# Kernel tuning notes

Measured on AMD Instinct MI355X. Metric: run time of the kernel, lower is better.

The kernel has to match this reference:

```python
import jax, jax.numpy as jnp
import numpy as np

N_IMAGES = 2  # matches init kwarg


def setup_inputs() -> dict:
    key = jax.random.key(0)
    x = jax.random.normal(key, (8192, 128), dtype=jnp.float32)
    return {"x": x}


def reference(x):
    n_images = N_IMAGES
    N, D = x.shape
    P = N // n_images  # number of 'persons'
    G = x @ x.T  # [N, N] pairwise dot products (Gram matrix)

    # Offset pairs (i<j) within a window of n_images consecutive indices.
    # NB: original code uses range(person, person + n_images) -> sliding window.
    offs = np.array([(i, j) for i in range(n_images) for j in range(i + 1, n_images)])
    oi = jnp.asarray(offs[:, 0])  # [k]
    oj = jnp.asarray(offs[:, 1])  # [k]
    k = offs.shape[0]  # C(n_images, 2)

    p = jnp.arange(P)
    self_i = p[:, None] + oi[None, :]  # [P, k]
    self_j = p[:, None] + oj[None, :]  # [P, k]
    sim_self = jnp.min(G[self_i, self_j], axis=1)  # [P] min over self pairs

    # Upper-triangular (i<j) values; mask everything else to -inf.
    neg = jnp.finfo(G.dtype).min
    rows = jnp.arange(N)
    upper = jnp.where(rows[:, None] < rows[None, :], G, neg)

    # similarity_oth[p] = max over all i<j pairs excluding person p's k self pairs.
    # Only the global top-(k+1) values can ever be that max.
    top_vals, top_idx = jax.lax.top_k(upper.reshape(-1), k + 1)  # [k+1]
    self_flat = self_i * N + self_j  # [P, k] flat indices of self pairs
    member = (top_idx[None, :, None] == self_flat[:, None, :]).any(-1)  # [P, k+1]
    sim_oth = jnp.max(jnp.where(member, neg, top_vals[None, :]), axis=1)  # [P]

    return jnp.mean(sim_oth / sim_self)
```

## Files before the change

kernel.cpp:

```cpp
#include <hip/hip_runtime.h>
#include <hip/hip_bf16.h>
#include <math.h>
#include <float.h>

static constexpr int NN    = 8192;
static constexpr int DD    = 128;
static constexpr int PP    = 4096;
static constexpr int TILE  = 128;
static constexpr int TT    = NN / TILE;
static constexpr int NBLK  = TT * (TT + 1) / 2;
static constexpr int NC    = NBLK * 2;
static constexpr int GRP   = 1088;
static constexpr int TLDS  = 16 * GRP;

struct Cand { float v; unsigned idx; };

using short8 = __attribute__((ext_vector_type(8))) short;
using f32x4  = __attribute__((ext_vector_type(4))) float;

typedef const __attribute__((address_space(1))) unsigned int* gas_uint;
typedef __attribute__((address_space(3))) unsigned int* las_uint;

__device__ __forceinline__ void dma16(const void* g, const void* l) {
    __builtin_amdgcn_global_load_lds(
        (gas_uint)(unsigned long long)g,
        (las_uint)(unsigned)(unsigned long long)l, 16, 0, 0);
}

__device__ __forceinline__ unsigned pk2(float lo, float hi) {
    unsigned a = (unsigned)__builtin_bit_cast(unsigned short, __float2bfloat16(lo));
    unsigned b = (unsigned)__builtin_bit_cast(unsigned short, __float2bfloat16(hi));
    return a | (b << 16);
}

__device__ __forceinline__ void push1(float& v1, unsigned& i1, float& v2, unsigned& i2,
                                      float w, unsigned j) {
    if (w > v1) { v2 = v1; i2 = i1; v1 = w; i1 = j; }
    else if (w > v2) { v2 = w; i2 = j; }
}

__device__ __forceinline__ void merge2(float& v1, unsigned& i1, float& v2, unsigned& i2,
                                       float w1, unsigned j1, float w2, unsigned j2) {
    if (w1 > v1) {
        float nv2; unsigned ni2;
        if (v1 >= w2) { nv2 = v1; ni2 = i1; } else { nv2 = w2; ni2 = j2; }
        v1 = w1; i1 = j1; v2 = nv2; i2 = ni2;
    } else if (w1 > v2) {
        v2 = w1; i2 = j1;
    }
}

__global__ __launch_bounds__(256) void k_prep(const float* __restrict__ x,
                                              unsigned short* __restrict__ xb,
                                              double* __restrict__ ss) {
    const int tid = threadIdx.x;
    if (blockIdx.x < 256) {
        int chunk = blockIdx.x * 256 + tid;
        const float4* s = (const float4*)(x + (size_t)chunk * 16);
        float4 f0 = s[0], f1 = s[1], f2 = s[2], f3 = s[3];
        uint4 o0 = {pk2(f0.x, f0.y), pk2(f0.z, f0.w), pk2(f1.x, f1.y), pk2(f1.z, f1.w)};
        uint4 o1 = {pk2(f2.x, f2.y), pk2(f2.z, f2.w), pk2(f3.x, f3.y), pk2(f3.z, f3.w)};
        uint4* d = (uint4*)(xb + (size_t)chunk * 16);
        d[0] = o0; d[1] = o1;
    } else {
        int b = blockIdx.x - 256;
        const int wv = tid >> 6, lane = tid & 63;
        #pragma unroll 4
        for (int u = 0; u < 16; ++u) {
            int p = b * 64 + wv * 16 + u;
            const float* a  = x + (size_t)p * DD;
            const float* bb = a + DD;
            double s = (double)a[lane] * (double)bb[lane]
                     + (double)a[lane + 64] * (double)bb[lane + 64];
            #pragma unroll
            for (int off = 32; off >= 1; off >>= 1) s += __shfl_down(s, off);
            if (lane == 0) ss[p] = s;
        }
    }
}

__global__ __launch_bounds__(256, 4) void k_top2(const unsigned short* __restrict__ xb,
                                                 Cand* __restrict__ cands) {
    __shared__ __align__(16) char AsB[TLDS];
    __shared__ __align__(16) char BsB[TLDS];
    __shared__ float sv1[4], sv2[4];
    __shared__ unsigned si1[4], si2[4];

    const int tid  = threadIdx.x;
    const int wv   = tid >> 6;
    const int lane = tid & 63;

    int rem = blockIdx.x;
    int ti = 0;
    while (rem >= TT - ti) { rem -= (TT - ti); ++ti; }
    int tj = ti + rem;

    const int wm   = wv >> 1;
    const int wn   = wv & 1;
    const int quad = lane >> 4;
    const int r16  = lane & 15;

    const int grow = lane >> 3;
    const int gcol = (lane & 7) * 8;

    f32x4 acc[4][4];
    #pragma unroll
    for (int mi = 0; mi < 4; ++mi)
        #pragma unroll
        for (int nj = 0; nj < 4; ++nj)
            acc[mi][nj] = (f32x4){0.f, 0.f, 0.f, 0.f};

    #pragma unroll
    for (int p = 0; p < 2; ++p) {
        const int kk = p * 64;
        if (p) __syncthreads();

        #pragma unroll
        for (int t = 0; t < 4; ++t) {
            int g = wv * 4 + t;
            const unsigned short* ga =
                xb + (size_t)(ti * TILE + g * 8 + grow) * DD + kk + gcol;
            dma16(ga, AsB + g * GRP);
            const unsigned short* gb =
                xb + (size_t)(tj * TILE + g * 8 + grow) * DD + kk + gcol;
            dma16(gb, BsB + g * GRP);
        }
        __syncthreads();

        #pragma unroll
        for (int s = 0; s < 2; ++s) {
            const int cc = quad + 4 * s;
            short8 af[4], bfr[4];
            #pragma unroll
            for (int mi = 0; mi < 4; ++mi) {
                int ra = wm * 64 + mi * 16 + r16;
                af[mi] = *(const short8*)(AsB + (ra >> 3) * GRP + (ra & 7) * 128 + cc * 16);
                int rb = wn * 64 + mi * 16 + r16;
                bfr[mi] = *(const short8*)(BsB + (rb >> 3) * GRP + (rb & 7) * 128 + cc * 16);
            }
            #pragma unroll
            for (int mi = 0; mi < 4; ++mi)
                #pragma unroll
                for (int nj = 0; nj < 4; ++nj)
                    acc[mi][nj] = __builtin_amdgcn_mfma_f32_16x16x32_bf16(
                        af[mi], bfr[nj], acc[mi][nj], 0, 0, 0);
        }
    }

    const int ibase = ti * TILE + wm * 64;
    const int jbase = tj * TILE + wn * 64;
    float v1 = -INFINITY, v2 = -INFINITY;
    unsigned i1 = 0, i2 = 0;
    #pragma unroll
    for (int mi = 0; mi < 4; ++mi) {
        #pragma unroll
        for (int nj = 0; nj < 4; ++nj) {
            int gj = jbase + nj * 16 + r16;
            #pragma unroll
            for (int reg = 0; reg < 4; ++reg) {
                int gi = ibase + mi * 16 + quad * 4 + reg;
                if (gi < gj) {
                    unsigned idx = (unsigned)(gi * NN + gj);
                    push1(v1, i1, v2, i2, acc[mi][nj][reg], idx);
                }
            }
        }
    }

    #pragma unroll
    for (int off = 32; off >= 1; off >>= 1) {
        float    w1 = __shfl_down(v1, off);
        unsigned j1 = (unsigned)__shfl_down((int)i1, off);
        float    w2 = __shfl_down(v2, off);
        unsigned j2 = (unsigned)__shfl_down((int)i2, off);
        merge2(v1, i1, v2, i2, w1, j1, w2, j2);
    }
    if (lane == 0) { sv1[wv] = v1; si1[wv] = i1; sv2[wv] = v2; si2[wv] = i2; }
    __syncthreads();
    if (tid == 0) {
        for (int w = 1; w < 4; ++w)
            merge2(v1, i1, v2, i2, sv1[w], si1[w], sv2[w], si2[w]);
        cands[blockIdx.x * 2]     = {v1, i1};
        cands[blockIdx.x * 2 + 1] = {v2, i2};
    }
}

__global__ __launch_bounds__(256) void k_final(const float* __restrict__ x,
                                               const double* __restrict__ ss,
                                               const Cand* __restrict__ cands,
                                               float* __restrict__ out) {
    __shared__ float redv[8];
    __shared__ float s_thresh;
    __shared__ int cnt;
    __shared__ unsigned qidx[128];
    __shared__ double qex[128];
    __shared__ double sd1, sd2;
    __shared__ unsigned stopi;
    __shared__ double sacc[256];

    const int tid  = threadIdx.x;
    const int wv   = tid >> 6;
    const int lane = tid & 63;
    if (tid == 0) cnt = 0;

    float v1 = -INFINITY, v2 = -INFINITY;
    for (int e = tid; e < NC; e += 256) {
        float v = cands[e].v;
        if (v > v1) { v2 = v1; v1 = v; }
        else if (v > v2) v2 = v;
    }
    #pragma unroll
    for (int off = 32; off >= 1; off >>= 1) {
        float w1 = __shfl_down(v1, off);
        float w2 = __shfl_down(v2, off);
        if (w1 > v1) { v2 = (v1 >= w2) ? v1 : w2; v1 = w1; }
        else if (w1 > v2) v2 = w1;
    }
    if (lane == 0) { redv[wv * 2] = v1; redv[wv * 2 + 1] = v2; }
    __syncthreads();
    if (tid == 0) {
        float a1 = -INFINITY, a2 = -INFINITY;
        for (int e = 0; e < 8; ++e) {
            float v = redv[e];
            if (v > a1) { a2 = a1; a1 = v; }
            else if (v > a2) a2 = v;
        }
        s_thresh = a2 - 1.0f;
    }
    __syncthreads();
    const float thresh = s_thresh;

    for (int e = tid; e < NC; e += 256) {
        if (cands[e].v >= thresh) {
            int k = atomicAdd(&cnt, 1);
            if (k < 128) qidx[k] = cands[e].idx;
        }
    }
    __syncthreads();
    const int n = cnt < 128 ? cnt : 128;

    for (int c = wv; c < n; c += 4) {
        unsigned idx = qidx[c];
        unsigned gi = idx >> 13;
        unsigned gj = idx & 8191;
        const float* pa = x + (size_t)gi * DD;
        const float* pb = x + (size_t)gj * DD;
        double s = (double)pa[lane] * (double)pb[lane]
                 + (double)pa[lane + 64] * (double)pb[lane + 64];
        #pragma unroll
        for (int off = 32; off >= 1; off >>= 1) s += __shfl_down(s, off);
        if (lane == 0) qex[c] = s;
    }
    __syncthreads();

    if (tid == 0) {
        double d1 = -DBL_MAX, d2 = -DBL_MAX;
        unsigned bi = 0;
        for (int c = 0; c < n; ++c) {
            double v = qex[c];
            if (v > d1) { d2 = d1; d1 = v; bi = qidx[c]; }
            else if (v > d2) d2 = v;
        }
        sd1 = d1; sd2 = d2; stopi = bi;
    }
    __syncthreads();

    const double top1 = sd1, top2 = sd2;
    const unsigned topi = stopi;

    double acc = 0.0;
    for (int p = tid; p < PP; p += 256) {
        unsigned selfidx = (unsigned)(p * NN + p + 1);
        double so = (topi == selfidx) ? top2 : top1;
        acc += so / ss[p];
    }
    sacc[tid] = acc;
    __syncthreads();
    for (int s = 128; s >= 1; s >>= 1) {
        if (tid < s) sacc[tid] += sacc[tid + s];
        __syncthreads();
    }
    if (tid == 0) out[0] = (float)(sacc[0] / (double)PP);
}

extern "C" void kernel_launch(void* const* d_in, const int* in_sizes, int n_in,
                              void* d_out, int out_size, void* d_ws, size_t ws_size,
                              hipStream_t stream) {
    (void)in_sizes; (void)n_in; (void)out_size; (void)ws_size;
    const float* x = (const float*)d_in[0];
    float* out = (float*)d_out;

    double* ss  = (double*)d_ws;
    Cand* cands = (Cand*)((char*)d_ws + PP * sizeof(double));
    unsigned short* xb = (unsigned short*)((char*)d_ws + 131072);

    k_prep<<<320, 256, 0, stream>>>(x, xb, ss);
    k_top2<<<NBLK, 256, 0, stream>>>(xb, cands);
    k_final<<<1, 256, 0, stream>>>(x, ss, cands, out);
}
```

Measured before the change: 174.9 us.

## Restructure Gram top-2 into persistent strips with register-resident A and double-buffered B

```diff
diff --git a/kernel.cpp b/kernel.cpp
--- a/kernel.cpp
+++ b/kernel.cpp
@@ -6,12 +6,8 @@
 static constexpr int NN    = 8192;
 static constexpr int DD    = 128;
 static constexpr int PP    = 4096;
-static constexpr int TILE  = 128;
-static constexpr int TT    = NN / TILE;
-static constexpr int NBLK  = TT * (TT + 1) / 2;
-static constexpr int NC    = NBLK * 2;
-static constexpr int GRP   = 1088;
-static constexpr int TLDS  = 16 * GRP;
+static constexpr int NBLK2 = 512;
+static constexpr int NC    = NBLK2 * 4 * 2;
 
 struct Cand { float v; unsigned idx; };
 
@@ -54,16 +50,15 @@
                                               unsigned short* __restrict__ xb,
                                               double* __restrict__ ss) {
     const int tid = threadIdx.x;
-    if (blockIdx.x < 256) {
-        int chunk = blockIdx.x * 256 + tid;
-        const float4* s = (const float4*)(x + (size_t)chunk * 16);
-        float4 f0 = s[0], f1 = s[1], f2 = s[2], f3 = s[3];
-        uint4 o0 = {pk2(f0.x, f0.y), pk2(f0.z, f0.w), pk2(f1.x, f1.y), pk2(f1.z, f1.w)};
-        uint4 o1 = {pk2(f2.x, f2.y), pk2(f2.z, f2.w), pk2(f3.x, f3.y), pk2(f3.z, f3.w)};
-        uint4* d = (uint4*)(xb + (size_t)chunk * 16);
-        d[0] = o0; d[1] = o1;
+    if (blockIdx.x < 512) {
+        int g = blockIdx.x * 256 + tid;
+        int r = g >> 4, c = g & 15;
+        const float4* s = (const float4*)(x + (size_t)g * 8);
+        float4 f0 = s[0], f1 = s[1];
+        uint4 o = {pk2(f0.x, f0.y), pk2(f0.z, f0.w), pk2(f1.x, f1.y), pk2(f1.z, f1.w)};
+        *(uint4*)((char*)xb + (size_t)r * 256 + ((c ^ (r & 7)) * 16)) = o;
     } else {
-        int b = blockIdx.x - 256;
+        int b = blockIdx.x - 512;
         const int wv = tid >> 6, lane = tid & 63;
         #pragma unroll 4
         for (int u = 0; u < 16; ++u) {
@@ -79,93 +74,101 @@
     }
 }
 
-__global__ __launch_bounds__(256, 4) void k_top2(const unsigned short* __restrict__ xb,
+__global__ __launch_bounds__(256, 2) void k_top2(const unsigned short* __restrict__ xb,
                                                  Cand* __restrict__ cands) {
-    __shared__ __align__(16) char AsB[TLDS];
-    __shared__ __align__(16) char BsB[TLDS];
-    __shared__ float sv1[4], sv2[4];
-    __shared__ unsigned si1[4], si2[4];
+    __shared__ __align__(16) char lds[4][2][8192];
 
     const int tid  = threadIdx.x;
     const int wv   = tid >> 6;
     const int lane = tid & 63;
-
-    int rem = blockIdx.x;
-    int ti = 0;
-    while (rem >= TT - ti) { rem -= (TT - ti); ++ti; }
-    int tj = ti + rem;
-
-    const int wm   = wv >> 1;
-    const int wn   = wv & 1;
     const int quad = lane >> 4;
     const int r16  = lane & 15;
-
-    const int grow = lane >> 3;
-    const int gcol = (lane & 7) * 8;
-
-    f32x4 acc[4][4];
-    #pragma unroll
-    for (int mi = 0; mi < 4; ++mi)
-        #pragma unroll
-        for (int nj = 0; nj < 4; ++nj)
-            acc[mi][nj] = (f32x4){0.f, 0.f, 0.f, 0.f};
-
-    #pragma unroll
-    for (int p = 0; p < 2; ++p) {
-        const int kk = p * 64;
-        if (p) __syncthreads();
-
-        #pragma unroll
-        for (int t = 0; t < 4; ++t) {
-            int g = wv * 4 + t;
-            const unsigned short* ga =
-                xb + (size_t)(ti * TILE + g * 8 + grow) * DD + kk + gcol;
-            dma16(ga, AsB + g * GRP);
-            const unsigned short* gb =
-                xb + (size_t)(tj * TILE + g * 8 + grow) * DD + kk + gcol;
-            dma16(gb, BsB + g * GRP);
-        }
-        __syncthreads();
-
-        #pragma unroll
-        for (int s = 0; s < 2; ++s) {
-            const int cc = quad + 4 * s;
-            short8 af[4], bfr[4];
-            #pragma unroll
-            for (int mi = 0; mi < 4; ++mi) {
-                int ra = wm * 64 + mi * 16 + r16;
-                af[mi] = *(const short8*)(AsB + (ra >> 3) * GRP + (ra & 7) * 128 + cc * 16);
-                int rb = wn * 64 + mi * 16 + r16;
-                bfr[mi] = *(const short8*)(BsB + (rb >> 3) * GRP + (rb & 7) * 128 + cc * 16);
-            }
-            #pragma unroll
-            for (int mi = 0; mi < 4; ++mi)
-                #pragma unroll
-                for (int nj = 0; nj < 4; ++nj)
-                    acc[mi][nj] = __builtin_amdgcn_mfma_f32_16x16x32_bf16(
-                        af[mi], bfr[nj], acc[mi][nj], 0, 0, 0);
-        }
-    }
-
-    const int ibase = ti * TILE + wm * 64;
-    const int jbase = tj * TILE + wn * 64;
+    const int k7   = r16 & 7;
+    char* buf = (char*)lds[wv];
+
+    const int p    = blockIdx.x >> 3;
+    const int sub  = blockIdx.x & 7;
+    const int v0   = sub * 8;
+    const int vend = (sub == 7) ? 65 : v0 + 8;
+    const int s0 = p, s1 = 127 - p;
+    const int L1 = 64 - (s0 >> 1);
+
+    #define SI_OF(v) (((v) < L1) ? s0 : s1)
+    #define TJ_OF(v) (((v) < L1) ? (s0 >> 1) + (v) : (s1 >> 1) + ((v) - L1))
+
+    {
+        const char* g = (const char*)xb + ((size_t)TJ_OF(v0) * 128 + wv * 32) * 256;
+        #pragma unroll
+        for (int t = 0; t < 8; ++t)
+            dma16(g + t * 1024 + (size_t)lane * 16, buf + t * 1024);
+    }
+
+    short8 af[4][4];
+    int cur_si = -1;
+
     float v1 = -INFINITY, v2 = -INFINITY;
     unsigned i1 = 0, i2 = 0;
-    #pragma unroll
-    for (int mi = 0; mi < 4; ++mi) {
-        #pragma unroll
-        for (int nj = 0; nj < 4; ++nj) {
-            int gj = jbase + nj * 16 + r16;
-            #pragma unroll
-            for (int reg = 0; reg < 4; ++reg) {
-                int gi = ibase + mi * 16 + quad * 4 + reg;
-                if (gi < gj) {
-                    unsigned idx = (unsigned)(gi * NN + gj);
-                    push1(v1, i1, v2, i2, acc[mi][nj][reg], idx);
+
+    for (int v = v0; v < vend; ++v) {
+        const int cur = (v - v0) & 1;
+        const int si  = SI_OF(v);
+        const int tj  = TJ_OF(v);
+
+        if (si != cur_si) {
+            cur_si = si;
+            const char* arow = (const char*)xb + ((size_t)si * 64 + r16) * 256;
+            #pragma unroll
+            for (int s = 0; s < 4; ++s)
+                #pragma unroll
+                for (int mi = 0; mi < 4; ++mi)
+                    af[s][mi] = *(const short8*)(arow + (size_t)(mi * 16) * 256
+                                                 + ((4 * s + quad) ^ k7) * 16);
+        }
+
+        if (v + 1 < vend) {
+            const char* g = (const char*)xb
+                          + ((size_t)TJ_OF(v + 1) * 128 + wv * 32) * 256;
+            char* nb = buf + (1 - cur) * 8192;
+            #pragma unroll
+            for (int t = 0; t < 8; ++t)
+                dma16(g + t * 1024 + (size_t)lane * 16, nb + t * 1024);
+            asm volatile("s_waitcnt vmcnt(8)" ::: "memory");
+        } else {
+            asm volatile("s_waitcnt vmcnt(0)" ::: "memory");
+        }
+
+        const char* cb = buf + cur * 8192;
+        short8 bfr[2][4];
+        #pragma unroll
+        for (int nj = 0; nj < 2; ++nj)
+            #pragma unroll
+            for (int s = 0; s < 4; ++s)
+                bfr[nj][s] = *(const short8*)(cb + (nj * 16 + r16) * 256
+                                              + ((4 * s + quad) ^ k7) * 16);
+
+        #pragma unroll
+        for (int mi = 0; mi < 4; ++mi) {
+            #pragma unroll
+            for (int nj = 0; nj < 2; ++nj) {
+                f32x4 a = __builtin_amdgcn_mfma_f32_16x16x32_bf16(
+                    af[0][mi], bfr[nj][0], (f32x4){0.f, 0.f, 0.f, 0.f}, 0, 0, 0);
+                #pragma unroll
+                for (int s = 1; s < 4; ++s)
+                    a = __builtin_amdgcn_mfma_f32_16x16x32_bf16(
+                        af[s][mi], bfr[nj][s], a, 0, 0, 0);
+                int gj  = tj * 128 + wv * 32 + nj * 16 + r16;
+                int gib = si * 64 + mi * 16 + quad * 4;
+                #pragma unroll
+                for (int reg = 0; reg < 4; ++reg) {
+                    int gi = gib + reg;
+                    if (gi < gj)
+                        push1(v1, i1, v2, i2, a[reg], (unsigned)(gi * NN + gj));
                 }
             }
         }
     }
+    #undef SI_OF
+    #undef TJ_OF
 
     #pragma unroll
     for (int off = 32; off >= 1; off >>= 1) {
@@ -175,13 +178,9 @@
         unsigned j2 = (unsigned)__shfl_down((int)i2, off);
         merge2(v1, i1, v2, i2, w1, j1, w2, j2);
     }
-    if (lane == 0) { sv1[wv] = v1; si1[wv] = i1; sv2[wv] = v2; si2[wv] = i2; }
-    __syncthreads();
-    if (tid == 0) {
-        for (int w = 1; w < 4; ++w)
-            merge2(v1, i1, v2, i2, sv1[w], si1[w], sv2[w], si2[w]);
-        cands[blockIdx.x * 2]     = {v1, i1};
-        cands[blockIdx.x * 2 + 1] = {v2, i2};
+    if (lane == 0) {
+        cands[(blockIdx.x * 4 + wv) * 2]     = {v1, i1};
+        cands[(blockIdx.x * 4 + wv) * 2 + 1] = {v2, i2};
     }
 }
 
@@ -291,10 +290,10 @@
     float* out = (float*)d_out;
 
     double* ss  = (double*)d_ws;
-    Cand* cands = (Cand*)((char*)d_ws + PP * sizeof(double));
+    Cand* cands = (Cand*)((char*)d_ws + 32768);
     unsigned short* xb = (unsigned short*)((char*)d_ws + 131072);
 
-    k_prep<<<320, 256, 0, stream>>>(x, xb, ss);
-    k_top2<<<NBLK, 256, 0, stream>>>(xb, cands);
+    k_prep<<<576, 256, 0, stream>>>(x, xb, ss);
+    k_top2<<<NBLK2, 256, 0, stream>>>(xb, cands);
     k_final<<<1, 256, 0, stream>>>(x, ss, cands, out);
 }
```

Measured after the change: 178.4 us. 2.0% more time.
